# Kernel optimization log

Hardware: AMD Instinct MI355X
Metric: run time of the kernel (lower is better)

The kernel has to match this reference:

```python
import jax, jax.numpy as jnp
import numpy as np

N = 50000
E = 800000
IN_DIM = 128
HID = 64
HEADS = 4
OUT_DIM = 128


def setup_inputs() -> dict:
    key = jax.random.key(0)
    ks = jax.random.split(key, 12)
    s = lambda fan: 1.0 / np.sqrt(fan)
    return {
        'features': jax.random.normal(ks[0], (N, IN_DIM), jnp.float32),
        'edge_index': jax.random.randint(ks[1], (2, E), 0, N, jnp.int64),
        # layer 1: in_dim -> heads*hid, concat=True
        'W1': jax.random.normal(ks[2], (IN_DIM, HEADS * HID), jnp.float32) * s(IN_DIM),
        'att_src1': jax.random.normal(ks[3], (HEADS, HID), jnp.float32) * s(HID),
        'att_dst1': jax.random.normal(ks[4], (HEADS, HID), jnp.float32) * s(HID),
        'bias1': jnp.zeros((HEADS * HID,), jnp.float32),
        # layer 2: heads*hid -> out_dim, 1 head, concat=False
        'W2': jax.random.normal(ks[5], (HEADS * HID, OUT_DIM), jnp.float32) * s(HEADS * HID),
        'att_src2': jax.random.normal(ks[6], (1, OUT_DIM), jnp.float32) * s(OUT_DIM),
        'att_dst2': jax.random.normal(ks[7], (1, OUT_DIM), jnp.float32) * s(OUT_DIM),
        'bias2': jnp.zeros((OUT_DIM,), jnp.float32),
    }


def _gat_conv(x, src, dst, W, a_src, a_dst, bias, heads, out_ch):
    n = x.shape[0]
    h = (x @ W).reshape(n, heads, out_ch)              # [N, H, C]
    alpha_s = jnp.einsum('nhc,hc->nh', h, a_src)       # [N, H]
    alpha_d = jnp.einsum('nhc,hc->nh', h, a_dst)
    e = jax.nn.leaky_relu(alpha_s[src] + alpha_d[dst], 0.2)  # [E, H]
    # segment softmax over incoming edges of each dst node
    m = jax.ops.segment_max(e, dst, num_segments=n)
    m = jnp.where(jnp.isfinite(m), m, 0.0)
    ex = jnp.exp(e - m[dst])
    denom = jax.ops.segment_sum(ex, dst, num_segments=n)
    alpha = ex / denom[dst]                            # [E, H]
    out = jax.ops.segment_sum(alpha[:, :, None] * h[src], dst, num_segments=n)  # [N, H, C]
    return out.reshape(n, heads * out_ch) + bias


def reference(features, edge_index, W1, att_src1, att_dst1, bias1, W2, att_src2, att_dst2, bias2):
    n = features.shape[0]
    loops = jnp.arange(n, dtype=edge_index.dtype)
    src = jnp.concatenate([edge_index[0], loops])
    dst = jnp.concatenate([edge_index[1], loops])

    act = lambda v: jax.nn.leaky_relu(v, 0.2)
    x = _gat_conv(features, src, dst, W1, att_src1, att_dst1, bias1, HEADS, HID)
    x = act(x)  # dropout inactive (eval)
    x = _gat_conv(x, src, dst, W2, att_src2, att_dst2, bias2, 1, OUT_DIM)
    x = act(x)
    # in_dim == out_dim -> identity residual
    return x + features
```

## Files before the change

### kernel.cpp

```cpp
#include <hip/hip_runtime.h>
#include <math.h>

#define LRELU(x) ((x) > 0.0f ? (x) : 0.2f * (x))

typedef __attribute__((ext_vector_type(8))) short bf16x8;
typedef __attribute__((ext_vector_type(4))) float floatx4;

__device__ __forceinline__ float bf2f(ushort u) {
    union { unsigned u; float f; } v; v.u = ((unsigned)u) << 16; return v.f;
}
__device__ __forceinline__ ushort f2bf(float f) {
    union { float f; unsigned u; } v; v.f = f;
    unsigned r = (v.u + 0x7FFFu + ((v.u >> 16) & 1u)) >> 16;
    return (ushort)r;
}

__global__ __launch_bounds__(256) void prep_kernel(
    const float* __restrict__ feat, const float* __restrict__ W1,
    const float* __restrict__ as1, const float* __restrict__ ad1,
    const float* __restrict__ W2, const float* __restrict__ as2,
    const float* __restrict__ ad2, const int* __restrict__ ei,
    ushort* __restrict__ featb, ushort* __restrict__ Bp1, ushort* __restrict__ Bp2,
    int* __restrict__ deg, ushort* __restrict__ col,
    int N, int E, int b_cvt, int b_p1, int b_p2)
{
    const int b = blockIdx.x, t = threadIdx.x;
    if (b < b_cvt) {
        int i = b * 256 + t;
        if (i < N * 32) {
            float4 v = ((const float4*)feat)[i];
            ushort4 o;
            o.x = f2bf(v.x); o.y = f2bf(v.y); o.z = f2bf(v.z); o.w = f2bf(v.w);
            ((ushort4*)featb)[i] = o;
        }
    } else if (b < b_cvt + b_p1) {
        int i = (b - b_cvt) * 256 + t;
        if (i < 272 * 128) {
            int n = i / 128, k = i % 128;
            float v;
            if (n < 256) v = W1[k * 256 + n];
            else if (n < 260) {
                int h = n - 256; float s = 0.f;
                for (int c = 0; c < 64; ++c) s += W1[k * 256 + h * 64 + c] * as1[h * 64 + c];
                v = s;
            } else if (n < 264) {
                int h = n - 260; float s = 0.f;
                for (int c = 0; c < 64; ++c) s += W1[k * 256 + h * 64 + c] * ad1[h * 64 + c];
                v = s;
            } else v = 0.f;
            Bp1[i] = f2bf(v);
        }
    } else if (b < b_cvt + b_p1 + b_p2) {
        int i = (b - b_cvt - b_p1) * 256 + t;
        if (i < 144 * 256) {
            int n = i / 256, k = i % 256;
            float v;
            if (n < 128) v = W2[k * 128 + n];
            else if (n == 128) {
                float s = 0.f;
                for (int c = 0; c < 128; ++c) s += W2[k * 128 + c] * as2[c];
                v = s;
            } else if (n == 129) {
                float s = 0.f;
                for (int c = 0; c < 128; ++c) s += W2[k * 128 + c] * ad2[c];
                v = s;
            } else v = 0.f;
            Bp2[i] = f2bf(v);
        }
    } else {
        const int base = (b - b_cvt - b_p1 - b_p2) * 1024;
        int srcs[4], dsts[4], slots[4];
        bool val[4];
#pragma unroll
        for (int q = 0; q < 4; ++q) {
            int k = base + q * 256 + t;
            val[q] = k < E;
            if (val[q]) { srcs[q] = ei[k]; dsts[q] = ei[E + k]; }
        }
#pragma unroll
        for (int q = 0; q < 4; ++q)
            if (val[q]) slots[q] = atomicAdd(&deg[dsts[q]], 1);
#pragma unroll
        for (int q = 0; q < 4; ++q)
            if (val[q] && slots[q] < 63) col[dsts[q] * 64 + slots[q]] = (ushort)srcs[q];
    }
}

__global__ __launch_bounds__(256) void gemm_attn1_kernel(
    const ushort* __restrict__ A, const ushort* __restrict__ Bp,
    float* __restrict__ as_, float* __restrict__ ad_, int M)
{
    const int lane = threadIdx.x & 63;
    const int wave = threadIdx.x >> 6;
    const int quad = lane >> 4;
    const int l16  = lane & 15;
    const int row0 = blockIdx.x * 64 + wave * 16;
    const int arow = min(row0 + l16, M - 1);
    const ushort* ap = A + (size_t)arow * 128 + quad * 8;
    const ushort* bp = Bp + (size_t)(256 + l16) * 128 + quad * 8;

    floatx4 acc = (floatx4){0.f, 0.f, 0.f, 0.f};
#pragma unroll
    for (int k0 = 0; k0 < 128; k0 += 32) {
        bf16x8 a = *(const bf16x8*)(ap + k0);
        bf16x8 b = *(const bf16x8*)(bp + k0);
        acc = __builtin_amdgcn_mfma_f32_16x16x32_bf16(a, b, acc, 0, 0, 0);
    }
#pragma unroll
    for (int r = 0; r < 4; ++r) {
        int row = row0 + quad * 4 + r;
        if (row < M) {
            float v = acc[r];
            if (l16 < 4)      as_[row * 4 + l16] = v;
            else if (l16 < 8) ad_[row * 4 + (l16 - 4)] = v;
        }
    }
}

__global__ __launch_bounds__(256) void gat_gather1_kernel(
    const int* __restrict__ deg, const ushort* __restrict__ col,
    const float* __restrict__ as_, const float* __restrict__ ad_,
    const ushort* __restrict__ xb, ushort* __restrict__ aggx, int N)
{
    __shared__ float4 alph[4][64];
    const int lane = threadIdx.x & 63;
    const int wave = threadIdx.x >> 6;
    const int n = blockIdx.x * 4 + wave;
    if (n >= N) return;
    const int dgE = min(deg[n], 63);
    const float4 ad4 = *(const float4*)(ad_ + n * 4);

    int src = n;
    float4 ex4 = {0.f, 0.f, 0.f, 0.f};
    if (lane <= dgE) {
        if (lane < dgE) src = col[n * 64 + lane];
        float4 a4 = *(const float4*)(as_ + src * 4);
        ex4.x = __expf(LRELU(a4.x + ad4.x));
        ex4.y = __expf(LRELU(a4.y + ad4.y));
        ex4.z = __expf(LRELU(a4.z + ad4.z));
        ex4.w = __expf(LRELU(a4.w + ad4.w));
        alph[wave][lane] = ex4;
    }
    float sx = ex4.x, sy = ex4.y, sz = ex4.z, sw = ex4.w;
#pragma unroll
    for (int m = 1; m < 64; m <<= 1) {
        sx += __shfl_xor(sx, m, 64); sy += __shfl_xor(sy, m, 64);
        sz += __shfl_xor(sz, m, 64); sw += __shfl_xor(sw, m, 64);
    }
    const float rd[4] = {1.0f / sx, 1.0f / sy, 1.0f / sz, 1.0f / sw};

    const int esl = lane >> 5;
    const int ch0 = (lane & 31) * 4;
    const int dg = dgE + 1;
    float acc[4][4] = {};
    for (int j0 = 0; j0 < dg; j0 += 8) {
        ushort4 u[4]; float4 a[4]; bool v[4]; int jj[4];
#pragma unroll
        for (int q = 0; q < 4; ++q) {
            jj[q] = j0 + 2 * q + esl;
            v[q] = jj[q] < dg;
            if (v[q]) {
                int s = __shfl(src, jj[q], 64);
                a[q] = alph[wave][jj[q]];
                u[q] = *(const ushort4*)(xb + (size_t)s * 128 + ch0);
            }
        }
#pragma unroll
        for (int q = 0; q < 4; ++q) {
            if (v[q]) {
                float f0 = bf2f(u[q].x), f1 = bf2f(u[q].y), f2 = bf2f(u[q].z), f3 = bf2f(u[q].w);
                acc[0][0] += a[q].x * f0; acc[0][1] += a[q].x * f1; acc[0][2] += a[q].x * f2; acc[0][3] += a[q].x * f3;
                acc[1][0] += a[q].y * f0; acc[1][1] += a[q].y * f1; acc[1][2] += a[q].y * f2; acc[1][3] += a[q].y * f3;
                acc[2][0] += a[q].z * f0; acc[2][1] += a[q].z * f1; acc[2][2] += a[q].z * f2; acc[2][3] += a[q].z * f3;
                acc[3][0] += a[q].w * f0; acc[3][1] += a[q].w * f1; acc[3][2] += a[q].w * f2; acc[3][3] += a[q].w * f3;
            }
        }
    }
#pragma unroll
    for (int h = 0; h < 4; ++h)
#pragma unroll
        for (int c = 0; c < 4; ++c) acc[h][c] += __shfl_xor(acc[h][c], 32, 64);

    if (lane < 32) {
#pragma unroll
        for (int h = 0; h < 4; ++h) {
            ushort4 o;
            o.x = f2bf(acc[h][0] * rd[h]); o.y = f2bf(acc[h][1] * rd[h]);
            o.z = f2bf(acc[h][2] * rd[h]); o.w = f2bf(acc[h][3] * rd[h]);
            *(ushort4*)(aggx + ((size_t)h * N + n) * 128 + ch0) = o;
        }
    }
}

__global__ __launch_bounds__(256) void gemm_head_kernel(
    const ushort* __restrict__ aggx, const ushort* __restrict__ Bp1,
    const float* __restrict__ bias, ushort* __restrict__ x1b, int M)
{
    const int h = blockIdx.y;
    const int lane = threadIdx.x & 63;
    const int wave = threadIdx.x >> 6;
    const int quad = lane >> 4;
    const int l16  = lane & 15;
    const int row0 = blockIdx.x * 64 + wave * 16;
    const int arow = min(row0 + l16, M - 1);
    const ushort* ap = aggx + ((size_t)h * M + arow) * 128 + quad * 8;

    floatx4 acc[4];
#pragma unroll
    for (int i = 0; i < 4; ++i) acc[i] = (floatx4){0.f, 0.f, 0.f, 0.f};

#pragma unroll
    for (int k0 = 0; k0 < 128; k0 += 32) {
        bf16x8 a = *(const bf16x8*)(ap + k0);
#pragma unroll
        for (int nt = 0; nt < 4; ++nt) {
            bf16x8 b = *(const bf16x8*)(Bp1 + (size_t)(h * 64 + nt * 16 + l16) * 128 + k0 + quad * 8);
            acc[nt] = __builtin_amdgcn_mfma_f32_16x16x32_bf16(a, b, acc[nt], 0, 0, 0);
        }
    }
#pragma unroll
    for (int nt = 0; nt < 4; ++nt) {
        float bv = bias[h * 64 + nt * 16 + l16];
#pragma unroll
        for (int r = 0; r < 4; ++r) {
            int row = row0 + quad * 4 + r;
            if (row < M) {
                float v = LRELU(acc[nt][r] + bv);
                x1b[(size_t)row * 256 + h * 64 + nt * 16 + l16] = f2bf(v);
            }
        }
    }
}

template <int K, int NTH, int H>
__global__ __launch_bounds__(256) void mfma_gemm_attn_kernel(
    const ushort* __restrict__ A, const ushort* __restrict__ Bp,
    ushort* __restrict__ Hout, float* __restrict__ as_, float* __restrict__ ad_, int M)
{
    constexpr int NT = NTH + 1;
    const int lane = threadIdx.x & 63;
    const int wave = threadIdx.x >> 6;
    const int quad = lane >> 4;
    const int l16  = lane & 15;
    const int row0 = blockIdx.x * 64 + wave * 16;
    const int arow = min(row0 + l16, M - 1);
    const ushort* ap = A + (size_t)arow * K + quad * 8;

    floatx4 acc[NT];
#pragma unroll
    for (int i = 0; i < NT; ++i) acc[i] = (floatx4){0.f, 0.f, 0.f, 0.f};

#pragma unroll
    for (int k0 = 0; k0 < K; k0 += 32) {
        bf16x8 a = *(const bf16x8*)(ap + k0);
#pragma unroll
        for (int nt = 0; nt < NT; ++nt) {
            bf16x8 b = *(const bf16x8*)(Bp + (size_t)(nt * 16 + l16) * K + k0 + quad * 8);
            acc[nt] = __builtin_amdgcn_mfma_f32_16x16x32_bf16(a, b, acc[nt], 0, 0, 0);
        }
    }
    constexpr int NCOL = NTH * 16;
#pragma unroll
    for (int nt = 0; nt < NTH; ++nt) {
#pragma unroll
        for (int r = 0; r < 4; ++r) {
            int row = row0 + quad * 4 + r;
            if (row < M) Hout[(size_t)row * NCOL + nt * 16 + l16] = f2bf(acc[nt][r]);
        }
    }
#pragma unroll
    for (int r = 0; r < 4; ++r) {
        int row = row0 + quad * 4 + r;
        if (row < M) {
            float v = acc[NTH][r];
            if (l16 < H)          as_[row * H + l16] = v;
            else if (l16 < 2 * H) ad_[row * H + (l16 - H)] = v;
        }
    }
}

__global__ __launch_bounds__(256) void gat_gather2_kernel(
    const int* __restrict__ deg, const ushort* __restrict__ col,
    const float* __restrict__ as_, const float* __restrict__ ad_,
    const ushort* __restrict__ h2, const float* __restrict__ bias,
    const float* __restrict__ resid, float* __restrict__ out, int N)
{
    __shared__ float alph[4][64];
    const int lane = threadIdx.x & 63;
    const int wave = threadIdx.x >> 6;
    const int n = blockIdx.x * 4 + wave;
    if (n >= N) return;
    const int dgE = min(deg[n], 63);
    const float adv = ad_[n];

    int src = n;
    float ex = 0.f;
    if (lane <= dgE) {
        if (lane < dgE) src = col[n * 64 + lane];
        ex = __expf(LRELU(as_[src] + adv));
        alph[wave][lane] = ex;
    }
    float s = ex;
#pragma unroll
    for (int m = 1; m < 64; m <<= 1) s += __shfl_xor(s, m, 64);
    const float rden = 1.0f / s;

    const int esl = lane >> 5;
    const int ch0 = (lane & 31) * 4;
    const int dg = dgE + 1;
    float ax = 0.f, ay = 0.f, az = 0.f, aw = 0.f;
    for (int j0 = 0; j0 < dg; j0 += 8) {
        ushort4 u[4]; float a[4]; bool v[4]; int jj[4];
#pragma unroll
        for (int q = 0; q < 4; ++q) {
            jj[q] = j0 + 2 * q + esl;
            v[q] = jj[q] < dg;
            if (v[q]) {
                int sA = __shfl(src, jj[q], 64);
                a[q] = alph[wave][jj[q]];
                u[q] = *(const ushort4*)(h2 + (size_t)sA * 128 + ch0);
            }
        }
#pragma unroll
        for (int q = 0; q < 4; ++q) {
            if (v[q]) {
                ax += a[q] * bf2f(u[q].x); ay += a[q] * bf2f(u[q].y);
                az += a[q] * bf2f(u[q].z); aw += a[q] * bf2f(u[q].w);
            }
        }
    }
    ax += __shfl_xor(ax, 32, 64); ay += __shfl_xor(ay, 32, 64);
    az += __shfl_xor(az, 32, 64); aw += __shfl_xor(aw, 32, 64);

    if (lane < 32) {
        const float4 bv = *(const float4*)(bias + ch0);
        const float4 fv = *(const float4*)(resid + (size_t)n * 128 + ch0);
        float4 o;
        o.x = LRELU(ax * rden + bv.x) + fv.x;
        o.y = LRELU(ay * rden + bv.y) + fv.y;
        o.z = LRELU(az * rden + bv.z) + fv.z;
        o.w = LRELU(aw * rden + bv.w) + fv.w;
        *(float4*)(out + (size_t)n * 128 + ch0) = o;
    }
}

extern "C" void kernel_launch(void* const* d_in, const int* in_sizes, int n_in,
                              void* d_out, int out_size, void* d_ws, size_t ws_size,
                              hipStream_t stream)
{
    const float* feat = (const float*)d_in[0];
    const int*   ei   = (const int*)d_in[1];
    const float* W1   = (const float*)d_in[2];
    const float* asrc1 = (const float*)d_in[3];
    const float* adst1 = (const float*)d_in[4];
    const float* bias1 = (const float*)d_in[5];
    const float* W2    = (const float*)d_in[6];
    const float* asrc2 = (const float*)d_in[7];
    const float* adst2 = (const float*)d_in[8];
    const float* bias2 = (const float*)d_in[9];
    float* outp = (float*)d_out;

    const int IN_DIM = 128, HC1 = 256, C2 = 128;
    const int N = in_sizes[0] / IN_DIM;
    const int E = in_sizes[1] / 2;

    char* w = (char*)d_ws;
    ushort* featb = (ushort*)w; w += (size_t)N * IN_DIM * 2;
    ushort* aggx  = (ushort*)w; w += (size_t)4 * N * IN_DIM * 2;
    ushort* x1b   = (ushort*)w; w += (size_t)N * HC1 * 2;
    ushort* h2b   = (ushort*)w; w += (size_t)N * C2 * 2;
    ushort* Bp1   = (ushort*)w; w += (size_t)272 * 128 * 2;
    ushort* Bp2   = (ushort*)w; w += (size_t)144 * 256 * 2;
    float* as1_   = (float*)w;  w += (size_t)N * 4 * 4;
    float* ad1_   = (float*)w;  w += (size_t)N * 4 * 4;
    float* as2_   = (float*)w;  w += (size_t)N * 4;
    float* ad2_   = (float*)w;  w += (size_t)N * 4;
    int* deg      = (int*)w;    w += (size_t)N * 4;
    ushort* col   = (ushort*)w; w += (size_t)N * 64 * 2;

    dim3 blk(256);
    const int mg = (N + 63) / 64;
    const int gg = (N + 3) / 4;

    const int b_cvt = (N * 32 + 255) / 256;
    const int b_p1  = (272 * 128 + 255) / 256;
    const int b_p2  = (144 * 256 + 255) / 256;
    const int b_fil = (E + 1023) / 1024;

    hipMemsetAsync(deg, 0, (size_t)N * 4, stream);
    prep_kernel<<<dim3(b_cvt + b_p1 + b_p2 + b_fil), blk, 0, stream>>>(
        feat, W1, asrc1, adst1, W2, asrc2, adst2, ei,
        featb, Bp1, Bp2, deg, col, N, E, b_cvt, b_p1, b_p2);

    gemm_attn1_kernel<<<dim3(mg), blk, 0, stream>>>(featb, Bp1, as1_, ad1_, N);
    gat_gather1_kernel<<<dim3(gg), blk, 0, stream>>>(deg, col, as1_, ad1_, featb, aggx, N);
    gemm_head_kernel<<<dim3(mg, 4), blk, 0, stream>>>(aggx, Bp1, bias1, x1b, N);

    mfma_gemm_attn_kernel<256, 8, 1><<<dim3(mg), blk, 0, stream>>>(x1b, Bp2, h2b, as2_, ad2_, N);
    gat_gather2_kernel<<<dim3(gg), blk, 0, stream>>>(deg, col, as2_, ad2_, h2b, bias2, feat, outp, N);
}
```

Before: 311.5 us.

## Fuse layer-1 head GEMM with layer-2 GEMM via LDS and partition CSR fill by dst

Merges the per-head output GEMM (with bias and leaky-relu) and the layer-2 projection/attention GEMM into one kernel. The intermediate x1 tile is kept in shared memory instead of written to and re-read from global memory, which also removes one launch. Separately, the edge-fill stage now splits destination nodes into 8 partitions. Each block scans 8192 edges and only handles those whose dst falls in its partition, so atomics and column writes land in a narrower address range. The cost is that every edge's dst is read 8 times, and the fused kernel has fewer blocks in flight with heavier register and LDS use.

```diff
diff --git a/kernel.cpp b/kernel.cpp
--- a/kernel.cpp
+++ b/kernel.cpp
@@ -22,7 +22,7 @@
     const float* __restrict__ ad2, const int* __restrict__ ei,
     ushort* __restrict__ featb, ushort* __restrict__ Bp1, ushort* __restrict__ Bp2,
     int* __restrict__ deg, ushort* __restrict__ col,
-    int N, int E, int b_cvt, int b_p1, int b_p2)
+    int N, int E, int Npart, int b_cvt, int b_p1, int b_p2)
 {
     const int b = blockIdx.x, t = threadIdx.x;
     if (b < b_cvt) {
@@ -68,21 +68,29 @@
             Bp2[i] = f2bf(v);
         }
     } else {
-        const int base = (b - b_cvt - b_p1 - b_p2) * 1024;
-        int srcs[4], dsts[4], slots[4];
-        bool val[4];
-#pragma unroll
-        for (int q = 0; q < 4; ++q) {
-            int k = base + q * 256 + t;
-            val[q] = k < E;
-            if (val[q]) { srcs[q] = ei[k]; dsts[q] = ei[E + k]; }
-        }
-#pragma unroll
-        for (int q = 0; q < 4; ++q)
-            if (val[q]) slots[q] = atomicAdd(&deg[dsts[q]], 1);
-#pragma unroll
-        for (int q = 0; q < 4; ++q)
-            if (val[q] && slots[q] < 63) col[dsts[q] * 64 + slots[q]] = (ushort)srcs[q];
+        const int fb = b - b_cvt - b_p1 - b_p2;
+        const int part = fb & 7;
+        const int base = (fb >> 3) * 8192;
+        const int lo = part * Npart;
+        const int hi = min(N, lo + Npart);
+        for (int q0 = 0; q0 < 32; q0 += 4) {
+            int dsts[4]; bool val[4];
+#pragma unroll
+            for (int u = 0; u < 4; ++u) {
+                int k = base + (q0 + u) * 256 + t;
+                val[u] = k < E;
+                if (val[u]) dsts[u] = ei[E + k];
+            }
+#pragma unroll
+            for (int u = 0; u < 4; ++u) {
+                if (val[u] && dsts[u] >= lo && dsts[u] < hi) {
+                    int k = base + (q0 + u) * 256 + t;
+                    int src = ei[k];
+                    int slot = atomicAdd(&deg[dsts[u]], 1);
+                    if (slot < 63) col[dsts[u] * 64 + slot] = (ushort)src;
+                }
+            }
+        }
     }
 }
 
@@ -192,89 +200,72 @@
     }
 }
 
-__global__ __launch_bounds__(256) void gemm_head_kernel(
+__global__ __launch_bounds__(256) void gemm_l1l2_kernel(
     const ushort* __restrict__ aggx, const ushort* __restrict__ Bp1,
-    const float* __restrict__ bias, ushort* __restrict__ x1b, int M)
-{
-    const int h = blockIdx.y;
+    const float* __restrict__ bias1, const ushort* __restrict__ Bp2,
+    ushort* __restrict__ h2b, float* __restrict__ as2_, float* __restrict__ ad2_, int M)
+{
+    __shared__ ushort x1s[64][264];
     const int lane = threadIdx.x & 63;
     const int wave = threadIdx.x >> 6;
     const int quad = lane >> 4;
     const int l16  = lane & 15;
     const int row0 = blockIdx.x * 64 + wave * 16;
     const int arow = min(row0 + l16, M - 1);
-    const ushort* ap = aggx + ((size_t)h * M + arow) * 128 + quad * 8;
-
-    floatx4 acc[4];
-#pragma unroll
-    for (int i = 0; i < 4; ++i) acc[i] = (floatx4){0.f, 0.f, 0.f, 0.f};
-
-#pragma unroll
-    for (int k0 = 0; k0 < 128; k0 += 32) {
-        bf16x8 a = *(const bf16x8*)(ap + k0);
+
+#pragma unroll
+    for (int h = 0; h < 4; ++h) {
+        const ushort* ap = aggx + ((size_t)h * M + arow) * 128 + quad * 8;
+        floatx4 acc[4];
+#pragma unroll
+        for (int i = 0; i < 4; ++i) acc[i] = (floatx4){0.f, 0.f, 0.f, 0.f};
+#pragma unroll
+        for (int k0 = 0; k0 < 128; k0 += 32) {
+            bf16x8 a = *(const bf16x8*)(ap + k0);
+#pragma unroll
+            for (int nt = 0; nt < 4; ++nt) {
+                bf16x8 b = *(const bf16x8*)(Bp1 + (size_t)(h * 64 + nt * 16 + l16) * 128 + k0 + quad * 8);
+                acc[nt] = __builtin_amdgcn_mfma_f32_16x16x32_bf16(a, b, acc[nt], 0, 0, 0);
+            }
+        }
 #pragma unroll
         for (int nt = 0; nt < 4; ++nt) {
-            bf16x8 b = *(const bf16x8*)(Bp1 + (size_t)(h * 64 + nt * 16 + l16) * 128 + k0 + quad * 8);
-            acc[nt] = __builtin_amdgcn_mfma_f32_16x16x32_bf16(a, b, acc[nt], 0, 0, 0);
-        }
-    }
-#pragma unroll
-    for (int nt = 0; nt < 4; ++nt) {
-        float bv = bias[h * 64 + nt * 16 + l16];
+            const int c = h * 64 + nt * 16 + l16;
+            const float bv = bias1[c];
+#pragma unroll
+            for (int r = 0; r < 4; ++r)
+                x1s[wave * 16 + quad * 4 + r][c] = f2bf(LRELU(acc[nt][r] + bv));
+        }
+    }
+    __syncthreads();
+
+    floatx4 acc2[9];
+#pragma unroll
+    for (int i = 0; i < 9; ++i) acc2[i] = (floatx4){0.f, 0.f, 0.f, 0.f};
+#pragma unroll
+    for (int k0 = 0; k0 < 256; k0 += 32) {
+        bf16x8 a = *(const bf16x8*)&x1s[wave * 16 + l16][k0 + quad * 8];
+#pragma unroll
+        for (int nt = 0; nt < 9; ++nt) {
+            bf16x8 b = *(const bf16x8*)(Bp2 + (size_t)(nt * 16 + l16) * 256 + k0 + quad * 8);
+            acc2[nt] = __builtin_amdgcn_mfma_f32_16x16x32_bf16(a, b, acc2[nt], 0, 0, 0);
+        }
+    }
+#pragma unroll
+    for (int nt = 0; nt < 8; ++nt) {
 #pragma unroll
         for (int r = 0; r < 4; ++r) {
             int row = row0 + quad * 4 + r;
-            if (row < M) {
-                float v = LRELU(acc[nt][r] + bv);
-                x1b[(size_t)row * 256 + h * 64 + nt * 16 + l16] = f2bf(v);
-            }
-        }
-    }
-}
-
-template <int K, int NTH, int H>
-__global__ __launch_bounds__(256) void mfma_gemm_attn_kernel(
-    const ushort* __restrict__ A, const ushort* __restrict__ Bp,
-    ushort* __restrict__ Hout, float* __restrict__ as_, float* __restrict__ ad_, int M)
-{
-    constexpr int NT = NTH + 1;
-    const int lane = threadIdx.x & 63;
-    const int wave = threadIdx.x >> 6;
-    const int quad = lane >> 4;
-    const int l16  = lane & 15;
-    const int row0 = blockIdx.x * 64 + wave * 16;
-    const int arow = min(row0 + l16, M - 1);
-    const ushort* ap = A + (size_t)arow * K + quad * 8;
-
-    floatx4 acc[NT];
-#pragma unroll
-    for (int i = 0; i < NT; ++i) acc[i] = (floatx4){0.f, 0.f, 0.f, 0.f};
-
-#pragma unroll
-    for (int k0 = 0; k0 < K; k0 += 32) {
-        bf16x8 a = *(const bf16x8*)(ap + k0);
-#pragma unroll
-        for (int nt = 0; nt < NT; ++nt) {
-            bf16x8 b = *(const bf16x8*)(Bp + (size_t)(nt * 16 + l16) * K + k0 + quad * 8);
-            acc[nt] = __builtin_amdgcn_mfma_f32_16x16x32_bf16(a, b, acc[nt], 0, 0, 0);
-        }
-    }
-    constexpr int NCOL = NTH * 16;
-#pragma unroll
-    for (int nt = 0; nt < NTH; ++nt) {
-#pragma unroll
-        for (int r = 0; r < 4; ++r) {
-            int row = row0 + quad * 4 + r;
-            if (row < M) Hout[(size_t)row * NCOL + nt * 16 + l16] = f2bf(acc[nt][r]);
+            if (row < M) h2b[(size_t)row * 128 + nt * 16 + l16] = f2bf(acc2[nt][r]);
         }
     }
 #pragma unroll
     for (int r = 0; r < 4; ++r) {
         int row = row0 + quad * 4 + r;
         if (row < M) {
-            float v = acc[NTH][r];
-            if (l16 < H)          as_[row * H + l16] = v;
-            else if (l16 < 2 * H) ad_[row * H + (l16 - H)] = v;
+            float v = acc2[8][r];
+            if (l16 == 0)      as2_[row] = v;
+            else if (l16 == 1) ad2_[row] = v;
         }
     }
 }
@@ -360,14 +351,13 @@
     const float* bias2 = (const float*)d_in[9];
     float* outp = (float*)d_out;
 
-    const int IN_DIM = 128, HC1 = 256, C2 = 128;
+    const int IN_DIM = 128, C2 = 128;
     const int N = in_sizes[0] / IN_DIM;
     const int E = in_sizes[1] / 2;
 
     char* w = (char*)d_ws;
     ushort* featb = (ushort*)w; w += (size_t)N * IN_DIM * 2;
     ushort* aggx  = (ushort*)w; w += (size_t)4 * N * IN_DIM * 2;
-    ushort* x1b   = (ushort*)w; w += (size_t)N * HC1 * 2;
     ushort* h2b   = (ushort*)w; w += (size_t)N * C2 * 2;
     ushort* Bp1   = (ushort*)w; w += (size_t)272 * 128 * 2;
     ushort* Bp2   = (ushort*)w; w += (size_t)144 * 256 * 2;
@@ -381,21 +371,22 @@
     dim3 blk(256);
     const int mg = (N + 63) / 64;
     const int gg = (N + 3) / 4;
+    const int Npart = (N + 7) / 8;
 
     const int b_cvt = (N * 32 + 255) / 256;
     const int b_p1  = (272 * 128 + 255) / 256;
     const int b_p2  = (144 * 256 + 255) / 256;
-    const int b_fil = (E + 1023) / 1024;
+    const int b_fil = 8 * ((E + 8191) / 8192);
 
     hipMemsetAsync(deg, 0, (size_t)N * 4, stream);
     prep_kernel<<<dim3(b_cvt + b_p1 + b_p2 + b_fil), blk, 0, stream>>>(
         feat, W1, asrc1, adst1, W2, asrc2, adst2, ei,
-        featb, Bp1, Bp2, deg, col, N, E, b_cvt, b_p1, b_p2);
+        featb, Bp1, Bp2, deg, col, N, E, Npart, b_cvt, b_p1, b_p2);
 
     gemm_attn1_kernel<<<dim3(mg), blk, 0, stream>>>(featb, Bp1, as1_, ad1_, N);
     gat_gather1_kernel<<<dim3(gg), blk, 0, stream>>>(deg, col, as1_, ad1_, featb, aggx, N);
-    gemm_head_kernel<<<dim3(mg, 4), blk, 0, stream>>>(aggx, Bp1, bias1, x1b, N);
-
-    mfma_gemm_attn_kernel<256, 8, 1><<<dim3(mg), blk, 0, stream>>>(x1b, Bp2, h2b, as2_, ad2_, N);
+
+    gemm_l1l2_kernel<<<dim3(mg), blk, 0, stream>>>(aggx, Bp1, bias1, Bp2, h2b, as2_, ad2_, N);
+
     gat_gather2_kernel<<<dim3(gg), blk, 0, stream>>>(deg, col, as2_, ad2_, h2b, bias2, feat, outp, N);
 }
```

Measured after the change: 305.2 us. -2.0%, faster.

## Partition edge-bucketing by destination range across eight block groups

Applied to the files above, without the earlier changes.

The CSR-style fill now splits destination nodes into eight ranges. Each fill block reads a chunk of 8192 dst indices and only performs the atomicAdd and col write for edges whose destination falls in its range. The aim is to localize atomic and scatter traffic (about 25 KB of deg per partition) so it stays in cache, and to cut contention across the whole grid. The cost is that every dst index is read eight times and each block does a serial loop over 32 edge groups.

```diff
diff --git a/kernel.cpp b/kernel.cpp
--- a/kernel.cpp
+++ b/kernel.cpp
@@ -22,7 +22,7 @@
     const float* __restrict__ ad2, const int* __restrict__ ei,
     ushort* __restrict__ featb, ushort* __restrict__ Bp1, ushort* __restrict__ Bp2,
     int* __restrict__ deg, ushort* __restrict__ col,
-    int N, int E, int b_cvt, int b_p1, int b_p2)
+    int N, int E, int Npart, int b_cvt, int b_p1, int b_p2)
 {
     const int b = blockIdx.x, t = threadIdx.x;
     if (b < b_cvt) {
@@ -68,21 +68,29 @@
             Bp2[i] = f2bf(v);
         }
     } else {
-        const int base = (b - b_cvt - b_p1 - b_p2) * 1024;
-        int srcs[4], dsts[4], slots[4];
-        bool val[4];
-#pragma unroll
-        for (int q = 0; q < 4; ++q) {
-            int k = base + q * 256 + t;
-            val[q] = k < E;
-            if (val[q]) { srcs[q] = ei[k]; dsts[q] = ei[E + k]; }
-        }
-#pragma unroll
-        for (int q = 0; q < 4; ++q)
-            if (val[q]) slots[q] = atomicAdd(&deg[dsts[q]], 1);
-#pragma unroll
-        for (int q = 0; q < 4; ++q)
-            if (val[q] && slots[q] < 63) col[dsts[q] * 64 + slots[q]] = (ushort)srcs[q];
+        const int fb = b - b_cvt - b_p1 - b_p2;
+        const int part = fb & 7;
+        const int base = (fb >> 3) * 8192;
+        const int lo = part * Npart;
+        const int hi = min(N, lo + Npart);
+        for (int q0 = 0; q0 < 32; q0 += 4) {
+            int dsts[4]; bool val[4];
+#pragma unroll
+            for (int u = 0; u < 4; ++u) {
+                int k = base + (q0 + u) * 256 + t;
+                val[u] = k < E;
+                if (val[u]) dsts[u] = ei[E + k];
+            }
+#pragma unroll
+            for (int u = 0; u < 4; ++u) {
+                if (val[u] && dsts[u] >= lo && dsts[u] < hi) {
+                    int k = base + (q0 + u) * 256 + t;
+                    int src = ei[k];
+                    int slot = atomicAdd(&deg[dsts[u]], 1);
+                    if (slot < 63) col[dsts[u] * 64 + slot] = (ushort)src;
+                }
+            }
+        }
     }
 }
 
@@ -381,16 +389,17 @@
     dim3 blk(256);
     const int mg = (N + 63) / 64;
     const int gg = (N + 3) / 4;
+    const int Npart = (N + 7) / 8;
 
     const int b_cvt = (N * 32 + 255) / 256;
     const int b_p1  = (272 * 128 + 255) / 256;
     const int b_p2  = (144 * 256 + 255) / 256;
-    const int b_fil = (E + 1023) / 1024;
+    const int b_fil = 8 * ((E + 8191) / 8192);
 
     hipMemsetAsync(deg, 0, (size_t)N * 4, stream);
     prep_kernel<<<dim3(b_cvt + b_p1 + b_p2 + b_fil), blk, 0, stream>>>(
         feat, W1, asrc1, adst1, W2, asrc2, adst2, ei,
-        featb, Bp1, Bp2, deg, col, N, E, b_cvt, b_p1, b_p2);
+        featb, Bp1, Bp2, deg, col, N, E, Npart, b_cvt, b_p1, b_p2);
 
     gemm_attn1_kernel<<<dim3(mg), blk, 0, stream>>>(featb, Bp1, as1_, ad1_, N);
     gat_gather1_kernel<<<dim3(gg), blk, 0, stream>>>(deg, col, as1_, ad1_, featb, aggx, N);
```

Result: no change. 307.1 us (-1.4%).
